# Kernel optimization log

Measured on AMD Instinct MI355X. Metric: run time of the kernel, lower is better.

The kernel has to match this reference:

```python
import jax, jax.numpy as jnp
import numpy as np
from jax import lax

P = (8, 10)        # partition size (p0, p1) for all four types
NUM_HEADS = 32
CURV = 1.0
EPS = 1e-5


def _ln(x, w, b):
    m = x.mean(-1, keepdims=True)
    v = ((x - m) ** 2).mean(-1, keepdims=True)
    return (x - m) / jnp.sqrt(v + EPS) * w + b


def _partition(x, p, mode):
    B, c, T, V = x.shape
    p0, p1 = p
    if mode == 1:
        y = x.reshape(B, c, T // p0, p0, V // p1, p1).transpose(0, 2, 4, 3, 5, 1)
    elif mode == 2:
        y = x.reshape(B, c, T // p0, p0, p1, V // p1).transpose(0, 2, 5, 3, 4, 1)
    elif mode == 3:
        y = x.reshape(B, c, p0, T // p0, V // p1, p1).transpose(0, 3, 4, 2, 5, 1)
    else:
        y = x.reshape(B, c, p0, T // p0, p1, V // p1).transpose(0, 3, 5, 2, 4, 1)
    return y.reshape(-1, p0, p1, c)


def _reverse(parts, B, TV, p, mode):
    T, V = TV
    p0, p1 = p
    y = parts.reshape(B, T // p0, V // p1, p0, p1, -1)
    perm = {1: (0, 5, 1, 3, 2, 4), 2: (0, 5, 1, 3, 4, 2),
            3: (0, 5, 3, 1, 2, 4), 4: (0, 5, 3, 1, 4, 2)}[mode]
    return y.transpose(perm).reshape(B, -1, T, V)


def _euc_to_poincare(x):
    n = jnp.maximum(jnp.linalg.norm(x, axis=-1, keepdims=True), 1e-10)
    return (-1.0 / CURV) * jnp.tanh(-CURV * n) * x / n


def _poincare_to_euc(x):
    n = jnp.clip(jnp.linalg.norm(x, axis=-1, keepdims=True), 1e-10, 1 - 1e-5)
    return jnp.arctanh(n * (-1.0 / CURV)) * x / n


def _linear_attention(x, h):
    # x: [Bw, N, 3*h*d]  (fused qkv channels)
    Bw, N, c3 = x.shape
    d = c3 // (3 * h)
    qkv = x.reshape(Bw, N, 3, h, d).transpose(2, 0, 3, 1, 4)  # [3,Bw,h,N,d]
    q = qkv[0] * (h ** -0.5)
    k, v = qkv[1], qkv[2]
    kv = jax.nn.softmax(jnp.einsum('bhnd,bhne->bhde', k, v), axis=-1)  # [Bw,h,d,d]
    attn = jnp.einsum('bhni,bhmi->bhnm', q, kv)                        # q @ kv^T
    return attn.transpose(0, 2, 1, 3).reshape(Bw, N, h * d)


def setup_inputs() -> dict:
    key = jax.random.key(0)
    ks = jax.random.split(key, 8)
    B, C, T, V = 32, 256, 64, 50
    s = 0.02
    return {
        'x': jax.random.normal(ks[0], (B, C, T, V), jnp.float32),
        'norm1_w': jnp.ones((C,), jnp.float32),
        'norm1_b': jnp.zeros((C,), jnp.float32),
        'map_w': jax.random.normal(ks[1], (C, 2 * C), jnp.float32) * s,
        'map_b': jnp.zeros((2 * C,), jnp.float32),
        'gconv': jax.random.normal(ks[2], (NUM_HEADS // 4, V, V), jnp.float32) * s,
        'tconv_w': jax.random.normal(ks[3], (C // 4, (C // 4) // (NUM_HEADS // 4), 7, 1), jnp.float32) * s,
        'tconv_b': jnp.zeros((C // 4,), jnp.float32),
        'proj_w': jax.random.normal(ks[4], (C, C), jnp.float32) * s,
        'proj_b': jnp.zeros((C,), jnp.float32),
        'norm2_w': jnp.ones((C,), jnp.float32),
        'norm2_b': jnp.zeros((C,), jnp.float32),
        'mlp_w1': jax.random.normal(ks[5], (C, 4 * C), jnp.float32) * s,
        'mlp_b1': jnp.zeros((4 * C,), jnp.float32),
        'mlp_w2': jax.random.normal(ks[6], (4 * C, C), jnp.float32) * s,
        'mlp_b2': jnp.zeros((C,), jnp.float32),
    }


def reference(x, norm1_w, norm1_b, map_w, map_b, gconv, tconv_w, tconv_b,
              proj_w, proj_b, norm2_w, norm2_b, mlp_w1, mlp_b1, mlp_w2, mlp_b2):
    B, C, T, V = x.shape
    xi = x.transpose(0, 2, 3, 1)                 # [B,T,V,C]
    skip = xi
    f = (_ln(xi, norm1_w, norm1_b) @ map_w + map_b).transpose(0, 3, 1, 2)  # [B,2C,T,V]
    f_conv, f_attn = f[:, :C // 2], f[:, C // 2:]
    fg, ft = f_conv[:, :C // 4], f_conv[:, C // 4:]
    G = gconv.shape[0]
    # learned graph conv over joints V (grouped over channels)
    y_g = jnp.einsum('bgctu,gvu->bgctv', fg.reshape(B, G, -1, T, V), gconv).reshape(B, -1, T, V)
    # grouped temporal conv (kernel_size x 1)
    y_t = lax.conv_general_dilated(ft, tconv_w, (1, 1), [(3, 3), (0, 0)],
                                   dimension_numbers=('NCHW', 'OIHW', 'NCHW'),
                                   feature_group_count=G) + tconv_b[None, :, None, None]
    ys = [y_g, y_t]
    ca = f_attn.shape[1] // 4                    # 3C/8 per branch (fused qkv)
    h = NUM_HEADS // 8
    for i in range(4):
        fa = f_attn[:, i * ca:(i + 1) * ca]
        parts = _partition(fa, P, i + 1).reshape(-1, P[0] * P[1], ca)
        a = _poincare_to_euc(_linear_attention(_euc_to_poincare(parts), h))
        ys.append(_reverse(a, B, (T, V), P, i + 1))
    out = jnp.concatenate(ys, axis=1).transpose(0, 2, 3, 1) @ proj_w + proj_b
    out = skip + out
    hmid = jax.nn.gelu(_ln(out, norm2_w, norm2_b) @ mlp_w1 + mlp_b1, approximate=False)
    out = out + (hmid @ mlp_w2 + mlp_b2)
    return out.transpose(0, 3, 1, 2)
```

## Files before the change

### kernel.cpp

```cpp
#include <hip/hip_runtime.h>
#include <hip/hip_bf16.h>
#include <math.h>

#define BB  32
#define TT  64
#define VV  50
#define TVV 3200

typedef __attribute__((ext_vector_type(8))) short s8v;
typedef __attribute__((ext_vector_type(4))) float f4v;

__device__ __forceinline__ unsigned short f2bf(float f) {
  __hip_bfloat16 h = __float2bfloat16(f);
  union { __hip_bfloat16 h; unsigned short u; } cv; cv.h = h; return cv.u;
}

#define LPITCH 40

template<int K>
__device__ __forceinline__ void gemm_core(const unsigned short* __restrict__ A,
                                          const unsigned short* __restrict__ B,
                                          int m0, int n0,
                                          unsigned short* sA, unsigned short* sB,
                                          f4v (&acc)[4][4]) {
  const int tid  = threadIdx.x;
  const int lane = tid & 63;
  const int wave = tid >> 6;
  const int wr = wave >> 1, wc = wave & 1;
  const int q = lane >> 4, l15 = lane & 15;
  const int row0 = tid >> 2;
  const int kq0  = (tid & 3) << 3;
  for (int k0 = 0; k0 < K; k0 += 32) {
#pragma unroll
    for (int i = 0; i < 2; ++i) {
      int row = row0 + i * 64;
      s8v av = *(const s8v*)(A + (size_t)(m0 + row) * K + k0 + kq0);
      s8v bv = *(const s8v*)(B + (size_t)(n0 + row) * K + k0 + kq0);
      *(s8v*)(sA + row * LPITCH + kq0) = av;
      *(s8v*)(sB + row * LPITCH + kq0) = bv;
    }
    __syncthreads();
    s8v af[4], bfr[4];
#pragma unroll
    for (int i = 0; i < 4; ++i) {
      af[i]  = *(const s8v*)(sA + (wr * 64 + i * 16 + l15) * LPITCH + q * 8);
      bfr[i] = *(const s8v*)(sB + (wc * 64 + i * 16 + l15) * LPITCH + q * 8);
    }
#pragma unroll
    for (int mi = 0; mi < 4; ++mi)
#pragma unroll
      for (int ni = 0; ni < 4; ++ni)
        acc[mi][ni] = __builtin_amdgcn_mfma_f32_16x16x32_bf16(af[mi], bfr[ni], acc[mi][ni], 0, 0, 0);
    __syncthreads();
  }
}

__global__ __launch_bounds__(256)
void k_wprep(const float* __restrict__ src, unsigned short* __restrict__ dst, int K, int N) {
  int idx = blockIdx.x * 256 + threadIdx.x;
  if (idx >= N * K) return;
  int n = idx / K, k = idx - n * K;
  dst[idx] = f2bf(src[(size_t)k * N + n]);
}

__global__ __launch_bounds__(256)
void k_xpose(const float* __restrict__ x, int b0, float* __restrict__ xtok) {
  __shared__ float sx[64][65];
  int m0 = blockIdx.x * 64;
  int c0 = blockIdx.y * 64;
  int b = b0 + m0 / TVV, tv0 = m0 % TVV;
  int tid = threadIdx.x;
  int tvi = tid & 63, ci = tid >> 6;
  const float* xb = x + ((size_t)b * 256 + c0) * TVV + tv0;
#pragma unroll
  for (int j = 0; j < 16; ++j) {
    int cc = ci + j * 4;
    sx[cc][tvi] = xb[(size_t)cc * TVV + tvi];
  }
  __syncthreads();
  int cj = tid & 63, rj = tid >> 6;
#pragma unroll
  for (int j = 0; j < 16; ++j) {
    int tv = rj + j * 4;
    xtok[(size_t)(m0 + tv) * 256 + c0 + cj] = sx[cj][tv];
  }
}

__global__ __launch_bounds__(256)
void k_ln(const float* __restrict__ src, const float* __restrict__ w, const float* __restrict__ b,
          unsigned short* __restrict__ dst) {
  int tid = threadIdx.x;
  int tk = tid >> 2, p = tid & 3;
  size_t m = (size_t)blockIdx.x * 64 + tk;
  const float4* row = (const float4*)(src + m * 256 + p * 64);
  float4 r[16];
  float s = 0.f, ss = 0.f;
#pragma unroll
  for (int j = 0; j < 16; ++j) {
    r[j] = row[j];
    s  += r[j].x + r[j].y + r[j].z + r[j].w;
    ss += r[j].x*r[j].x + r[j].y*r[j].y + r[j].z*r[j].z + r[j].w*r[j].w;
  }
  __shared__ float sb1[256], sb2[256];
  sb1[tid] = s; sb2[tid] = ss;
  __syncthreads();
  int base = tk << 2;
  s  = sb1[base] + sb1[base+1] + sb1[base+2] + sb1[base+3];
  ss = sb2[base] + sb2[base+1] + sb2[base+2] + sb2[base+3];
  float mu = s * (1.f / 256.f);
  float rstd = rsqrtf(ss * (1.f / 256.f) - mu * mu + 1e-5f);
  ushort4* drow = (ushort4*)(dst + m * 256 + p * 64);
#pragma unroll
  for (int j = 0; j < 16; ++j) {
    int c = p * 64 + j * 4;
    ushort4 o;
    o.x = f2bf((r[j].x - mu) * rstd * w[c]     + b[c]);
    o.y = f2bf((r[j].y - mu) * rstd * w[c + 1] + b[c + 1]);
    o.z = f2bf((r[j].z - mu) * rstd * w[c + 2] + b[c + 2]);
    o.w = f2bf((r[j].w - mu) * rstd * w[c + 3] + b[c + 3]);
    drow[j] = o;
  }
}

__global__ __launch_bounds__(256)
void k_gemm_map(const unsigned short* __restrict__ xln, const unsigned short* __restrict__ wT,
                const float* __restrict__ bias, float* __restrict__ f) {
  __shared__ __align__(16) unsigned short sm[2 * 128 * LPITCH];
  int m0 = blockIdx.x * 128, n0 = blockIdx.y * 128;
  f4v acc[4][4];
#pragma unroll
  for (int i = 0; i < 4; ++i)
#pragma unroll
    for (int j = 0; j < 4; ++j) acc[i][j] = (f4v){0.f, 0.f, 0.f, 0.f};
  gemm_core<256>(xln, wT, m0, n0, sm, sm + 128 * LPITCH, acc);
  const int tid = threadIdx.x, lane = tid & 63, wave = tid >> 6;
  const int wr = wave >> 1, wc = wave & 1, q = lane >> 4, l15 = lane & 15;
#pragma unroll
  for (int ni = 0; ni < 4; ++ni) {
    int n = n0 + wc * 64 + ni * 16 + l15;
    float bz = bias[n];
#pragma unroll
    for (int mi = 0; mi < 4; ++mi) {
      int m = m0 + wr * 64 + mi * 16 + q * 4;
#pragma unroll
      for (int rr = 0; rr < 4; ++rr)
        f[(size_t)(m + rr) * 512 + n] = acc[mi][ni][rr] + bz;
    }
  }
}

__global__ __launch_bounds__(256)
void k_gemm_proj(const unsigned short* __restrict__ ycat, const unsigned short* __restrict__ wT,
                 const float* __restrict__ bias, float* __restrict__ out1) {
  __shared__ __align__(16) unsigned short sm[2 * 128 * LPITCH];
  int m0 = blockIdx.x * 128, n0 = blockIdx.y * 128;
  f4v acc[4][4];
#pragma unroll
  for (int i = 0; i < 4; ++i)
#pragma unroll
    for (int j = 0; j < 4; ++j) acc[i][j] = (f4v){0.f, 0.f, 0.f, 0.f};
  gemm_core<256>(ycat, wT, m0, n0, sm, sm + 128 * LPITCH, acc);
  const int tid = threadIdx.x, lane = tid & 63, wave = tid >> 6;
  const int wr = wave >> 1, wc = wave & 1, q = lane >> 4, l15 = lane & 15;
#pragma unroll
  for (int ni = 0; ni < 4; ++ni) {
    int n = n0 + wc * 64 + ni * 16 + l15;
    float bz = bias[n];
#pragma unroll
    for (int mi = 0; mi < 4; ++mi) {
      int m = m0 + wr * 64 + mi * 16 + q * 4;
#pragma unroll
      for (int rr = 0; rr < 4; ++rr) {
        size_t idx = (size_t)(m + rr) * 256 + n;
        out1[idx] = out1[idx] + acc[mi][ni][rr] + bz;
      }
    }
  }
}

__global__ __launch_bounds__(256)
void k_gemm_mlp1(const unsigned short* __restrict__ xln2, const unsigned short* __restrict__ wT,
                 const float* __restrict__ bias, unsigned short* __restrict__ hmid) {
  __shared__ __align__(16) unsigned short sm[2 * 128 * LPITCH];
  int m0 = blockIdx.x * 128, n0 = blockIdx.y * 128;
  f4v acc[4][4];
#pragma unroll
  for (int i = 0; i < 4; ++i)
#pragma unroll
    for (int j = 0; j < 4; ++j) acc[i][j] = (f4v){0.f, 0.f, 0.f, 0.f};
  gemm_core<256>(xln2, wT, m0, n0, sm, sm + 128 * LPITCH, acc);
  const int tid = threadIdx.x, lane = tid & 63, wave = tid >> 6;
  const int wr = wave >> 1, wc = wave & 1, q = lane >> 4, l15 = lane & 15;
#pragma unroll
  for (int ni = 0; ni < 4; ++ni) {
    int n = n0 + wc * 64 + ni * 16 + l15;
    float bz = bias[n];
#pragma unroll
    for (int mi = 0; mi < 4; ++mi) {
      int m = m0 + wr * 64 + mi * 16 + q * 4;
#pragma unroll
      for (int rr = 0; rr < 4; ++rr) {
        float h = acc[mi][ni][rr] + bz;
        float g = 0.5f * h * (1.f + erff(h * 0.70710678118654752f));
        hmid[(size_t)(m + rr) * 1024 + n] = f2bf(g);
      }
    }
  }
}

__global__ __launch_bounds__(256)
void k_gemm_mlp2(const unsigned short* __restrict__ hmid, const unsigned short* __restrict__ wT,
                 const float* __restrict__ bias, const float* __restrict__ out1,
                 float* __restrict__ out, int b0) {
  __shared__ __align__(16) unsigned short sm[2 * 128 * LPITCH];
  int m0 = blockIdx.x * 128, n0 = blockIdx.y * 128;
  f4v acc[4][4];
#pragma unroll
  for (int i = 0; i < 4; ++i)
#pragma unroll
    for (int j = 0; j < 4; ++j) acc[i][j] = (f4v){0.f, 0.f, 0.f, 0.f};
  gemm_core<1024>(hmid, wT, m0, n0, sm, sm + 128 * LPITCH, acc);
  const int tid = threadIdx.x, lane = tid & 63, wave = tid >> 6;
  const int wr = wave >> 1, wc = wave & 1, q = lane >> 4, l15 = lane & 15;
  float* twv = (float*)sm + wave * 16 * 65;
  int mbase = m0 + wr * 64;
  int bglob = b0 + mbase / TVV;
  int tvb = mbase % TVV;
  for (int ni = 0; ni < 4; ++ni) {
    int n = n0 + wc * 64 + ni * 16 + l15;
    float bz = bias[n];
#pragma unroll
    for (int mi = 0; mi < 4; ++mi) {
      int ml = mi * 16 + q * 4;
#pragma unroll
      for (int rr = 0; rr < 4; ++rr) {
        int m = mbase + ml + rr;
        twv[l15 * 65 + ml + rr] = acc[mi][ni][rr] + bz + out1[(size_t)m * 256 + n];
      }
    }
    __syncthreads();
#pragma unroll
    for (int np = 0; np < 16; ++np) {
      int n2 = n0 + wc * 64 + ni * 16 + np;
      out[((size_t)bglob * 256 + n2) * TVV + tvb + lane] = twv[np * 65 + lane];
    }
    __syncthreads();
  }
}

__global__ __launch_bounds__(256)
void k_gconv(const float* __restrict__ f, const float* __restrict__ gw,
             unsigned short* __restrict__ ycat) {
  __shared__ float sf[50][64];
  int bc = blockIdx.x >> 6, t = blockIdx.x & 63;
  int tid = threadIdx.x;
  size_t tok0 = (size_t)bc * TVV + t * 50;
  for (int idx = tid; idx < 3200; idx += 256) {
    int u = idx >> 6, oc = idx & 63;
    sf[u][oc] = f[(tok0 + u) * 512 + oc];
  }
  __syncthreads();
  for (int idx = tid; idx < 3200; idx += 256) {
    int v = idx >> 6, oc = idx & 63;
    const float* gr = gw + ((size_t)(oc >> 3) * 50 + v) * 50;
    float s = 0.f;
#pragma unroll 10
    for (int u = 0; u < 50; ++u) s += sf[u][oc] * gr[u];
    ycat[(tok0 + v) * 256 + oc] = f2bf(s);
  }
}

__global__ __launch_bounds__(256)
void k_tconv(const float* __restrict__ f, const float* __restrict__ tw,
             const float* __restrict__ tb, unsigned short* __restrict__ ycat) {
  __shared__ float sw[64 * 57];
  int bc = blockIdx.x >> 6, t = blockIdx.x & 63;
  int tid = threadIdx.x;
  for (int idx = tid; idx < 64 * 56; idx += 256) {
    int oc = idx / 56, k = idx - oc * 56;
    sw[oc * 57 + k] = tw[idx];
  }
  __syncthreads();
  size_t base = (size_t)bc * TVV;
  for (int idx = tid; idx < 3200; idx += 256) {
    int v = idx >> 6, oc = idx & 63;
    int g = oc >> 3;
    float s = tb[oc];
#pragma unroll
    for (int kt = 0; kt < 7; ++kt) {
      int ts = t + kt - 3;
      if (ts < 0 || ts >= 64) continue;
      const float* fr = f + (base + ts * 50 + v) * 512 + 64 + g * 8;
      const float* wr_ = sw + oc * 57 + kt;
#pragma unroll
      for (int ic = 0; ic < 8; ++ic) s += fr[ic] * wr_[ic * 7];
    }
    ycat[(base + t * 50 + v) * 256 + 64 + oc] = f2bf(s);
  }
}

__global__ __launch_bounds__(256)
void k_attn(const float* __restrict__ f, unsigned short* __restrict__ ycat) {
  int mode = blockIdx.z, bc = blockIdx.y;
  int wt = blockIdx.x / 5, wv = blockIdx.x % 5;
  __shared__ float parts[80][97];
  __shared__ float kvb[256];
  __shared__ float obuf[80][33];
  __shared__ float scl[80];
  int tid = threadIdx.x;
  size_t base = (size_t)bc * TVV;
  int ch0 = 128 + mode * 96;
  for (int idx = tid; idx < 80 * 96; idx += 256) {
    int n = idx / 96, ch = idx - n * 96;
    int lt = n / 10, lv = n - lt * 10;
    int t = (mode < 2) ? (wt * 8 + lt) : (lt * 8 + wt);
    int v = ((mode & 1) == 0) ? (wv * 10 + lv) : (lv * 5 + wv);
    parts[n][ch] = f[(base + t * 50 + v) * 512 + ch0 + ch];
  }
  __syncthreads();
  if (tid < 80) {
    float s = 0.f;
    for (int ch = 0; ch < 96; ++ch) { float val = parts[tid][ch]; s += val * val; }
    float nrm = fmaxf(sqrtf(s), 1e-10f);
    float sc = tanhf(nrm) / nrm;
    for (int ch = 0; ch < 96; ++ch) parts[tid][ch] *= sc;
  }
  __syncthreads();
  {
    int h = tid >> 6, dd = (tid >> 3) & 7, e = tid & 7;
    float s = 0.f;
    for (int n = 0; n < 80; ++n)
      s += parts[n][32 + h * 8 + dd] * parts[n][64 + h * 8 + e];
    kvb[tid] = s;
  }
  __syncthreads();
  if (tid < 32) {
    int h = tid >> 3, dd = tid & 7;
    float* r = &kvb[h * 64 + dd * 8];
    float mx = r[0];
    for (int e = 1; e < 8; ++e) mx = fmaxf(mx, r[e]);
    float ex[8]; float sm2 = 0.f;
    for (int e = 0; e < 8; ++e) { ex[e] = expf(r[e] - mx); sm2 += ex[e]; }
    float inv = 1.f / sm2;
    for (int e = 0; e < 8; ++e) r[e] = ex[e] * inv;
  }
  __syncthreads();
  for (int idx = tid; idx < 80 * 32; idx += 256) {
    int n = idx >> 5, cc = idx & 31;
    int h = cc >> 3, m_ = cc & 7;
    float s = 0.f;
#pragma unroll
    for (int i = 0; i < 8; ++i)
      s += parts[n][h * 8 + i] * kvb[h * 64 + m_ * 8 + i];
    obuf[n][cc] = s * 0.5f;
  }
  __syncthreads();
  if (tid < 80) {
    float s = 0.f;
    for (int cc = 0; cc < 32; ++cc) { float val = obuf[tid][cc]; s += val * val; }
    float nn = sqrtf(s);
    nn = fminf(fmaxf(nn, 1e-10f), 1.f - 1e-5f);
    scl[tid] = -atanhf(nn) / nn;
  }
  __syncthreads();
  for (int idx = tid; idx < 80 * 32; idx += 256) {
    int n = idx >> 5, cc = idx & 31;
    int lt = n / 10, lv = n - lt * 10;
    int t = (mode < 2) ? (wt * 8 + lt) : (lt * 8 + wt);
    int v = ((mode & 1) == 0) ? (wv * 10 + lv) : (lv * 5 + wv);
    ycat[(base + t * 50 + v) * 256 + 128 + mode * 32 + cc] = f2bf(obuf[n][cc] * scl[n]);
  }
}

extern "C" void kernel_launch(void* const* d_in, const int* in_sizes, int n_in,
                              void* d_out, int out_size, void* d_ws, size_t ws_size,
                              hipStream_t stream) {
  const float* x       = (const float*)d_in[0];
  const float* n1w     = (const float*)d_in[1];
  const float* n1b     = (const float*)d_in[2];
  const float* map_w   = (const float*)d_in[3];
  const float* map_b   = (const float*)d_in[4];
  const float* gconv   = (const float*)d_in[5];
  const float* tconv_w = (const float*)d_in[6];
  const float* tconv_b = (const float*)d_in[7];
  const float* proj_w  = (const float*)d_in[8];
  const float* proj_b  = (const float*)d_in[9];
  const float* n2w     = (const float*)d_in[10];
  const float* n2b     = (const float*)d_in[11];
  const float* w1      = (const float*)d_in[12];
  const float* b1      = (const float*)d_in[13];
  const float* w2      = (const float*)d_in[14];
  const float* b2      = (const float*)d_in[15];
  float* out = (float*)d_out;

  const size_t WB = (size_t)(512 * 256 + 256 * 256 + 1024 * 256 + 256 * 1024) * 2;
  int CH = 32;
  while (CH > 1 && (size_t)CH * TVV * 4096 + WB > ws_size) CH >>= 1;
  if ((size_t)CH * TVV * 4096 + WB > ws_size) return;
  const int Mc = CH * TVV;
  const int nch = BB / CH;

  char* ws = (char*)d_ws;
  float* xtok            = (float*)ws;
  float* f               = (float*)(ws + (size_t)Mc * 1024);
  unsigned short* hmid   = (unsigned short*)f;
  unsigned short* xln    = (unsigned short*)(ws + (size_t)Mc * 3072);
  unsigned short* ycat   = (unsigned short*)(ws + (size_t)Mc * 3584);
  unsigned short* wmapT  = (unsigned short*)(ws + (size_t)Mc * 4096);
  unsigned short* wprojT = wmapT + 512 * 256;
  unsigned short* w1T    = wprojT + 256 * 256;
  unsigned short* w2T    = w1T + 1024 * 256;

  k_wprep<<<dim3((512 * 256 + 255) / 256), 256, 0, stream>>>(map_w, wmapT, 256, 512);
  k_wprep<<<dim3((256 * 256 + 255) / 256), 256, 0, stream>>>(proj_w, wprojT, 256, 256);
  k_wprep<<<dim3((1024 * 256 + 255) / 256), 256, 0, stream>>>(w1, w1T, 256, 1024);
  k_wprep<<<dim3((256 * 1024 + 255) / 256), 256, 0, stream>>>(w2, w2T, 1024, 256);

  for (int c = 0; c < nch; ++c) {
    int b0 = c * CH;
    k_xpose<<<dim3(CH * 50, 4), 256, 0, stream>>>(x, b0, xtok);
    k_ln<<<dim3(Mc / 64), 256, 0, stream>>>(xtok, n1w, n1b, xln);
    k_gemm_map<<<dim3(CH * 25, 4), 256, 0, stream>>>(xln, wmapT, map_b, f);
    k_gconv<<<dim3(CH * 64), 256, 0, stream>>>(f, gconv, ycat);
    k_tconv<<<dim3(CH * 64), 256, 0, stream>>>(f, tconv_w, tconv_b, ycat);
    k_attn<<<dim3(40, CH, 4), 256, 0, stream>>>(f, ycat);
    k_gemm_proj<<<dim3(CH * 25, 2), 256, 0, stream>>>(ycat, wprojT, proj_b, xtok);
    k_ln<<<dim3(Mc / 64), 256, 0, stream>>>(xtok, n2w, n2b, xln);
    k_gemm_mlp1<<<dim3(CH * 25, 8), 256, 0, stream>>>(xln, w1T, b1, hmid);
    k_gemm_mlp2<<<dim3(CH * 25, 2), 256, 0, stream>>>(hmid, w2T, b2, xtok, out, b0);
  }
}
```

Measured before the change: 1.068 ms.

## Fuse transpose with first LayerNorm, store map output as bf16, use LDS DMA loads

Merges the input transpose and the first LayerNorm into one kernel that reads x once and writes both the fp32 token copy and the bf16 normalized activations. The map GEMM now writes its output f in bf16 instead of fp32, which halves the traffic that gconv, tconv and attention read. The GEMM core now loads tiles with global_load_lds straight into an unpadded shared-memory layout, skipping the register round trip. The extra bf16 rounding of f lowers precision, and dropping the padding may cause LDS bank conflicts on the fragment reads.

Measured after the change: 1.003 ms. -6.1%, faster.

```diff
diff --git a/kernel.cpp b/kernel.cpp
--- a/kernel.cpp
+++ b/kernel.cpp
@@ -3,48 +3,50 @@
 #include <math.h>
 
 #define BB  32
-#define TT  64
-#define VV  50
 #define TVV 3200
+#define XB  819200
 
 typedef __attribute__((ext_vector_type(8))) short s8v;
 typedef __attribute__((ext_vector_type(4))) float f4v;
-
-__device__ __forceinline__ unsigned short f2bf(float f) {
+typedef unsigned short u16;
+typedef unsigned int   u32;
+
+__device__ __forceinline__ u16 f2bf(float f) {
   __hip_bfloat16 h = __float2bfloat16(f);
-  union { __hip_bfloat16 h; unsigned short u; } cv; cv.h = h; return cv.u;
-}
-
-#define LPITCH 40
+  union { __hip_bfloat16 h; u16 u; } cv; cv.h = h; return cv.u;
+}
+__device__ __forceinline__ float bf2f(u16 u) {
+  return __uint_as_float(((u32)u) << 16);
+}
+
+__device__ __forceinline__ void glds16(const u16* g, u16* l) {
+  __builtin_amdgcn_global_load_lds((const __attribute__((address_space(1))) u32*)g,
+                                   (__attribute__((address_space(3))) u32*)l, 16, 0, 0);
+}
 
 template<int K>
-__device__ __forceinline__ void gemm_core(const unsigned short* __restrict__ A,
-                                          const unsigned short* __restrict__ B,
-                                          int m0, int n0,
-                                          unsigned short* sA, unsigned short* sB,
-                                          f4v (&acc)[4][4]) {
-  const int tid  = threadIdx.x;
-  const int lane = tid & 63;
-  const int wave = tid >> 6;
+__device__ __forceinline__ void gemm_core(const u16* __restrict__ A, const u16* __restrict__ B,
+                                          int m0, int n0, u16* sA, u16* sB, f4v (&acc)[4][4]) {
+  const int tid = threadIdx.x, lane = tid & 63, wave = tid >> 6;
   const int wr = wave >> 1, wc = wave & 1;
   const int q = lane >> 4, l15 = lane & 15;
-  const int row0 = tid >> 2;
-  const int kq0  = (tid & 3) << 3;
+  const int srow = lane >> 2;
+  const int skq  = (lane & 3) << 3;
+  const u16* gA = A + (size_t)(m0 + wave * 32 + srow) * K + skq;
+  const u16* gB = B + (size_t)(n0 + wave * 32 + srow) * K + skq;
+  u16* lA = sA + wave * 1024;
+  u16* lB = sB + wave * 1024;
   for (int k0 = 0; k0 < K; k0 += 32) {
-#pragma unroll
-    for (int i = 0; i < 2; ++i) {
-      int row = row0 + i * 64;
-      s8v av = *(const s8v*)(A + (size_t)(m0 + row) * K + k0 + kq0);
-      s8v bv = *(const s8v*)(B + (size_t)(n0 + row) * K + k0 + kq0);
-      *(s8v*)(sA + row * LPITCH + kq0) = av;
-      *(s8v*)(sB + row * LPITCH + kq0) = bv;
-    }
+    glds16(gA + k0,                 lA);
+    glds16(gA + k0 + (size_t)16 * K, lA + 512);
+    glds16(gB + k0,                 lB);
+    glds16(gB + k0 + (size_t)16 * K, lB + 512);
     __syncthreads();
     s8v af[4], bfr[4];
 #pragma unroll
     for (int i = 0; i < 4; ++i) {
-      af[i]  = *(const s8v*)(sA + (wr * 64 + i * 16 + l15) * LPITCH + q * 8);
-      bfr[i] = *(const s8v*)(sB + (wc * 64 + i * 16 + l15) * LPITCH + q * 8);
+      af[i]  = *(const s8v*)(sA + (wr * 64 + i * 16 + l15) * 32 + q * 8);
+      bfr[i] = *(const s8v*)(sB + (wc * 64 + i * 16 + l15) * 32 + q * 8);
     }
 #pragma unroll
     for (int mi = 0; mi < 4; ++mi)
@@ -56,7 +58,7 @@
 }
 
 __global__ __launch_bounds__(256)
-void k_wprep(const float* __restrict__ src, unsigned short* __restrict__ dst, int K, int N) {
+void k_wprep(const float* __restrict__ src, u16* __restrict__ dst, int K, int N) {
   int idx = blockIdx.x * 256 + threadIdx.x;
   if (idx >= N * K) return;
   int n = idx / K, k = idx - n * K;
@@ -64,31 +66,51 @@
 }
 
 __global__ __launch_bounds__(256)
-void k_xpose(const float* __restrict__ x, int b0, float* __restrict__ xtok) {
-  __shared__ float sx[64][65];
-  int m0 = blockIdx.x * 64;
-  int c0 = blockIdx.y * 64;
+void k_lnx(const float* __restrict__ x, int b0, const float* __restrict__ w,
+           const float* __restrict__ bias, float* __restrict__ xtok, u16* __restrict__ xln) {
+  __shared__ float sx[32][264];
+  __shared__ float srs_[32][33], srq_[32][33];
+  __shared__ float smu[32], sst[32];
+  int m0 = blockIdx.x * 32;
   int b = b0 + m0 / TVV, tv0 = m0 % TVV;
   int tid = threadIdx.x;
-  int tvi = tid & 63, ci = tid >> 6;
-  const float* xb = x + ((size_t)b * 256 + c0) * TVV + tv0;
-#pragma unroll
-  for (int j = 0; j < 16; ++j) {
-    int cc = ci + j * 4;
-    sx[cc][tvi] = xb[(size_t)cc * TVV + tvi];
-  }
-  __syncthreads();
-  int cj = tid & 63, rj = tid >> 6;
-#pragma unroll
-  for (int j = 0; j < 16; ++j) {
-    int tv = rj + j * 4;
-    xtok[(size_t)(m0 + tv) * 256 + c0 + cj] = sx[cj][tv];
+  int qd = tid & 7, c = tid >> 3;
+  const float* xb = x + (size_t)b * XB + tv0;
+  float wreg = w[tid], breg = bias[tid];
+  float s[4] = {0.f, 0.f, 0.f, 0.f}, ss[4] = {0.f, 0.f, 0.f, 0.f};
+#pragma unroll
+  for (int k = 0; k < 8; ++k) {
+    int cc = k * 32 + c;
+    float4 vv = *(const float4*)(xb + (size_t)cc * TVV + qd * 4);
+    sx[qd * 4 + 0][cc] = vv.x; sx[qd * 4 + 1][cc] = vv.y;
+    sx[qd * 4 + 2][cc] = vv.z; sx[qd * 4 + 3][cc] = vv.w;
+    s[0] += vv.x; s[1] += vv.y; s[2] += vv.z; s[3] += vv.w;
+    ss[0] += vv.x * vv.x; ss[1] += vv.y * vv.y; ss[2] += vv.z * vv.z; ss[3] += vv.w * vv.w;
+  }
+#pragma unroll
+  for (int i = 0; i < 4; ++i) { srs_[qd * 4 + i][c] = s[i]; srq_[qd * 4 + i][c] = ss[i]; }
+  __syncthreads();
+  if (tid < 32) {
+    float t1 = 0.f, t2 = 0.f;
+#pragma unroll
+    for (int j = 0; j < 32; ++j) { t1 += srs_[tid][j]; t2 += srq_[tid][j]; }
+    float mu = t1 * (1.f / 256.f);
+    smu[tid] = mu;
+    sst[tid] = rsqrtf(t2 * (1.f / 256.f) - mu * mu + 1e-5f);
+  }
+  __syncthreads();
+  for (int tok = 0; tok < 32; ++tok) {
+    float val = sx[tok][tid];
+    float mu = smu[tok], rs = sst[tok];
+    size_t m = (size_t)(m0 + tok) * 256 + tid;
+    xtok[m] = val;
+    xln[m]  = f2bf((val - mu) * rs * wreg + breg);
   }
 }
 
 __global__ __launch_bounds__(256)
 void k_ln(const float* __restrict__ src, const float* __restrict__ w, const float* __restrict__ b,
-          unsigned short* __restrict__ dst) {
+          u16* __restrict__ dst) {
   int tid = threadIdx.x;
   int tk = tid >> 2, p = tid & 3;
   size_t m = (size_t)blockIdx.x * 64 + tk;
@@ -123,16 +145,16 @@
 }
 
 __global__ __launch_bounds__(256)
-void k_gemm_map(const unsigned short* __restrict__ xln, const unsigned short* __restrict__ wT,
-                const float* __restrict__ bias, float* __restrict__ f) {
-  __shared__ __align__(16) unsigned short sm[2 * 128 * LPITCH];
+void k_gemm_map(const u16* __restrict__ xln, const u16* __restrict__ wT,
+                const float* __restrict__ bias, u16* __restrict__ f) {
+  __shared__ __align__(16) u16 sm[8192];
   int m0 = blockIdx.x * 128, n0 = blockIdx.y * 128;
   f4v acc[4][4];
 #pragma unroll
   for (int i = 0; i < 4; ++i)
 #pragma unroll
     for (int j = 0; j < 4; ++j) acc[i][j] = (f4v){0.f, 0.f, 0.f, 0.f};
-  gemm_core<256>(xln, wT, m0, n0, sm, sm + 128 * LPITCH, acc);
+  gemm_core<256>(xln, wT, m0, n0, sm, sm + 4096, acc);
   const int tid = threadIdx.x, lane = tid & 63, wave = tid >> 6;
   const int wr = wave >> 1, wc = wave & 1, q = lane >> 4, l15 = lane & 15;
 #pragma unroll
@@ -144,22 +166,22 @@
       int m = m0 + wr * 64 + mi * 16 + q * 4;
 #pragma unroll
       for (int rr = 0; rr < 4; ++rr)
-        f[(size_t)(m + rr) * 512 + n] = acc[mi][ni][rr] + bz;
-    }
-  }
-}
-
-__global__ __launch_bounds__(256)
-void k_gemm_proj(const unsigned short* __restrict__ ycat, const unsigned short* __restrict__ wT,
+        f[(size_t)(m + rr) * 512 + n] = f2bf(acc[mi][ni][rr] + bz);
+    }
+  }
+}
+
+__global__ __launch_bounds__(256)
+void k_gemm_proj(const u16* __restrict__ ycat, const u16* __restrict__ wT,
                  const float* __restrict__ bias, float* __restrict__ out1) {
-  __shared__ __align__(16) unsigned short sm[2 * 128 * LPITCH];
+  __shared__ __align__(16) u16 sm[8192];
   int m0 = blockIdx.x * 128, n0 = blockIdx.y * 128;
   f4v acc[4][4];
 #pragma unroll
   for (int i = 0; i < 4; ++i)
 #pragma unroll
     for (int j = 0; j < 4; ++j) acc[i][j] = (f4v){0.f, 0.f, 0.f, 0.f};
-  gemm_core<256>(ycat, wT, m0, n0, sm, sm + 128 * LPITCH, acc);
+  gemm_core<256>(ycat, wT, m0, n0, sm, sm + 4096, acc);
   const int tid = threadIdx.x, lane = tid & 63, wave = tid >> 6;
   const int wr = wave >> 1, wc = wave & 1, q = lane >> 4, l15 = lane & 15;
 #pragma unroll
@@ -179,16 +201,16 @@
 }
 
 __global__ __launch_bounds__(256)
-void k_gemm_mlp1(const unsigned short* __restrict__ xln2, const unsigned short* __restrict__ wT,
-                 const float* __restrict__ bias, unsigned short* __restrict__ hmid) {
-  __shared__ __align__(16) unsigned short sm[2 * 128 * LPITCH];
+void k_gemm_mlp1(const u16* __restrict__ xln2, const u16* __restrict__ wT,
+                 const float* __restrict__ bias, u16* __restrict__ hmid) {
+  __shared__ __align__(16) u16 sm[8192];
   int m0 = blockIdx.x * 128, n0 = blockIdx.y * 128;
   f4v acc[4][4];
 #pragma unroll
   for (int i = 0; i < 4; ++i)
 #pragma unroll
     for (int j = 0; j < 4; ++j) acc[i][j] = (f4v){0.f, 0.f, 0.f, 0.f};
-  gemm_core<256>(xln2, wT, m0, n0, sm, sm + 128 * LPITCH, acc);
+  gemm_core<256>(xln2, wT, m0, n0, sm, sm + 4096, acc);
   const int tid = threadIdx.x, lane = tid & 63, wave = tid >> 6;
   const int wr = wave >> 1, wc = wave & 1, q = lane >> 4, l15 = lane & 15;
 #pragma unroll
@@ -209,17 +231,17 @@
 }
 
 __global__ __launch_bounds__(256)
-void k_gemm_mlp2(const unsigned short* __restrict__ hmid, const unsigned short* __restrict__ wT,
+void k_gemm_mlp2(const u16* __restrict__ hmid, const u16* __restrict__ wT,
                  const float* __restrict__ bias, const float* __restrict__ out1,
                  float* __restrict__ out, int b0) {
-  __shared__ __align__(16) unsigned short sm[2 * 128 * LPITCH];
+  __shared__ __align__(16) u16 sm[10240];
   int m0 = blockIdx.x * 128, n0 = blockIdx.y * 128;
   f4v acc[4][4];
 #pragma unroll
   for (int i = 0; i < 4; ++i)
 #pragma unroll
     for (int j = 0; j < 4; ++j) acc[i][j] = (f4v){0.f, 0.f, 0.f, 0.f};
-  gemm_core<1024>(hmid, wT, m0, n0, sm, sm + 128 * LPITCH, acc);
+  gemm_core<1024>(hmid, wT, m0, n0, sm, sm + 4096, acc);
   const int tid = threadIdx.x, lane = tid & 63, wave = tid >> 6;
   const int wr = wave >> 1, wc = wave & 1, q = lane >> 4, l15 = lane & 15;
   float* twv = (float*)sm + wave * 16 * 65;
@@ -249,15 +271,15 @@
 }
 
 __global__ __launch_bounds__(256)
-void k_gconv(const float* __restrict__ f, const float* __restrict__ gw,
-             unsigned short* __restrict__ ycat) {
+void k_gconv(const u16* __restrict__ f, const float* __restrict__ gw,
+             u16* __restrict__ ycat) {
   __shared__ float sf[50][64];
   int bc = blockIdx.x >> 6, t = blockIdx.x & 63;
   int tid = threadIdx.x;
   size_t tok0 = (size_t)bc * TVV + t * 50;
   for (int idx = tid; idx < 3200; idx += 256) {
     int u = idx >> 6, oc = idx & 63;
-    sf[u][oc] = f[(tok0 + u) * 512 + oc];
+    sf[u][oc] = bf2f(f[(tok0 + u) * 512 + oc]);
   }
   __syncthreads();
   for (int idx = tid; idx < 3200; idx += 256) {
@@ -271,8 +293,8 @@
 }
 
 __global__ __launch_bounds__(256)
-void k_tconv(const float* __restrict__ f, const float* __restrict__ tw,
-             const float* __restrict__ tb, unsigned short* __restrict__ ycat) {
+void k_tconv(const u16* __restrict__ f, const float* __restrict__ tw,
+             const float* __restrict__ tb, u16* __restrict__ ycat) {
   __shared__ float sw[64 * 57];
   int bc = blockIdx.x >> 6, t = blockIdx.x & 63;
   int tid = threadIdx.x;
@@ -290,17 +312,17 @@
     for (int kt = 0; kt < 7; ++kt) {
       int ts = t + kt - 3;
       if (ts < 0 || ts >= 64) continue;
-      const float* fr = f + (base + ts * 50 + v) * 512 + 64 + g * 8;
+      s8v fv = *(const s8v*)(f + (base + ts * 50 + v) * 512 + 64 + g * 8);
       const float* wr_ = sw + oc * 57 + kt;
 #pragma unroll
-      for (int ic = 0; ic < 8; ++ic) s += fr[ic] * wr_[ic * 7];
+      for (int ic = 0; ic < 8; ++ic) s += bf2f((u16)fv[ic]) * wr_[ic * 7];
     }
     ycat[(base + t * 50 + v) * 256 + 64 + oc] = f2bf(s);
   }
 }
 
 __global__ __launch_bounds__(256)
-void k_attn(const float* __restrict__ f, unsigned short* __restrict__ ycat) {
+void k_attn(const u16* __restrict__ f, u16* __restrict__ ycat) {
   int mode = blockIdx.z, bc = blockIdx.y;
   int wt = blockIdx.x / 5, wv = blockIdx.x % 5;
   __shared__ float parts[80][97];
@@ -315,7 +337,7 @@
     int lt = n / 10, lv = n - lt * 10;
     int t = (mode < 2) ? (wt * 8 + lt) : (lt * 8 + wt);
     int v = ((mode & 1) == 0) ? (wv * 10 + lv) : (lv * 5 + wv);
-    parts[n][ch] = f[(base + t * 50 + v) * 512 + ch0 + ch];
+    parts[n][ch] = bf2f(f[(base + t * 50 + v) * 512 + ch0 + ch]);
   }
   __syncthreads();
   if (tid < 80) {
@@ -401,32 +423,31 @@
   const int nch = BB / CH;
 
   char* ws = (char*)d_ws;
-  float* xtok            = (float*)ws;
-  float* f               = (float*)(ws + (size_t)Mc * 1024);
-  unsigned short* hmid   = (unsigned short*)f;
-  unsigned short* xln    = (unsigned short*)(ws + (size_t)Mc * 3072);
-  unsigned short* ycat   = (unsigned short*)(ws + (size_t)Mc * 3584);
-  unsigned short* wmapT  = (unsigned short*)(ws + (size_t)Mc * 4096);
-  unsigned short* wprojT = wmapT + 512 * 256;
-  unsigned short* w1T    = wprojT + 256 * 256;
-  unsigned short* w2T    = w1T + 1024 * 256;
-
-  k_wprep<<<dim3((512 * 256 + 255) / 256), 256, 0, stream>>>(map_w, wmapT, 256, 512);
-  k_wprep<<<dim3((256 * 256 + 255) / 256), 256, 0, stream>>>(proj_w, wprojT, 256, 256);
-  k_wprep<<<dim3((1024 * 256 + 255) / 256), 256, 0, stream>>>(w1, w1T, 256, 1024);
-  k_wprep<<<dim3((256 * 1024 + 255) / 256), 256, 0, stream>>>(w2, w2T, 1024, 256);
+  float* xtok   = (float*)ws;
+  u16* f        = (u16*)(ws + (size_t)Mc * 1024);
+  u16* hmid     = f;
+  u16* xln      = (u16*)(ws + (size_t)Mc * 3072);
+  u16* ycat     = (u16*)(ws + (size_t)Mc * 3584);
+  u16* wmapT    = (u16*)(ws + (size_t)Mc * 4096);
+  u16* wprojT   = wmapT + 512 * 256;
+  u16* w1T      = wprojT + 256 * 256;
+  u16* w2T      = w1T + 1024 * 256;
+
+  k_wprep<<<dim3(512), 256, 0, stream>>>(map_w, wmapT, 256, 512);
+  k_wprep<<<dim3(256), 256, 0, stream>>>(proj_w, wprojT, 256, 256);
+  k_wprep<<<dim3(1024), 256, 0, stream>>>(w1, w1T, 256, 1024);
+  k_wprep<<<dim3(1024), 256, 0, stream>>>(w2, w2T, 1024, 256);
 
   for (int c = 0; c < nch; ++c) {
     int b0 = c * CH;
-    k_xpose<<<dim3(CH * 50, 4), 256, 0, stream>>>(x, b0, xtok);
-    k_ln<<<dim3(Mc / 64), 256, 0, stream>>>(xtok, n1w, n1b, xln);
-    k_gemm_map<<<dim3(CH * 25, 4), 256, 0, stream>>>(xln, wmapT, map_b, f);
+    k_lnx<<<dim3(Mc / 32), 256, 0, stream>>>(x, b0, n1w, n1b, xtok, xln);
+    k_gemm_map<<<dim3(Mc / 128, 4), 256, 0, stream>>>(xln, wmapT, map_b, f);
     k_gconv<<<dim3(CH * 64), 256, 0, stream>>>(f, gconv, ycat);
     k_tconv<<<dim3(CH * 64), 256, 0, stream>>>(f, tconv_w, tconv_b, ycat);
     k_attn<<<dim3(40, CH, 4), 256, 0, stream>>>(f, ycat);
-    k_gemm_proj<<<dim3(CH * 25, 2), 256, 0, stream>>>(ycat, wprojT, proj_b, xtok);
+    k_gemm_proj<<<dim3(Mc / 128, 2), 256, 0, stream>>>(ycat, wprojT, proj_b, xtok);
     k_ln<<<dim3(Mc / 64), 256, 0, stream>>>(xtok, n2w, n2b, xln);
-    k_gemm_mlp1<<<dim3(CH * 25, 8), 256, 0, stream>>>(xln, w1T, b1, hmid);
-    k_gemm_mlp2<<<dim3(CH * 25, 2), 256, 0, stream>>>(hmid, w2T, b2, xtok, out, b0);
-  }
-}
+    k_gemm_mlp1<<<dim3(Mc / 128, 8), 256, 0, stream>>>(xln, w1T, b1, hmid);
+    k_gemm_mlp2<<<dim3(Mc / 128, 2), 256, 0, stream>>>(hmid, w2T, b2, xtok, out, b0);
+  }
+}
```
